# Performance work log

Hardware: AMD Instinct MI355X
Metric: run time of the kernel (lower is better)

The kernel has to match this reference:

```python
import jax, jax.numpy as jnp
import numpy as np

# dims
B, S, V, H, D, I, L, SL, P = 1, 2048, 32000, 1024, 512, 4096, 2, 32, 4096
DECAY_FAST, DECAY_SLOW, CONS_RATE, CONS_EVERY = 0.9, 0.99, 0.1, 10


def _ln(x, g, b):
    m = x.mean(-1, keepdims=True)
    v = ((x - m) ** 2).mean(-1, keepdims=True)
    return (x - m) * jax.lax.rsqrt(v + 1e-5) * g + b


def _memory_scan(items, gates, fast0, slow0):
    # items [B,S,D], gates [B,S,SL]; sequential per-timestep memory update
    cons = (jnp.arange(items.shape[1]) % CONS_EVERY) == 0
    def step(carry, x):
        fast, slow = carry
        item, gate, c = x
        fast = DECAY_FAST * fast + gate[:, :, None] * item[:, None, :]
        slow = jnp.where(c, DECAY_SLOW * slow + CONS_RATE * fast, slow)
        fast = jnp.where(c, (1.0 - CONS_RATE) * fast, fast)
        return (fast, slow), None
    (fast, slow), _ = jax.lax.scan(
        step, (fast0, slow0),
        (items.transpose(1, 0, 2), gates.transpose(1, 0, 2), cons))
    return fast, slow


def _forward(input_ids, fast_states, slow_states, emb, pos_emb, W_item, b_item,
             W_q, b_q, rh_W1, rh_b1, rh_W2, rh_b2, gate_W, gate_b, W_out, b_out,
             ln1_g, ln1_b, ffn_W1, ffn_b1, ffn_W2, ffn_b2, ln2_g, ln2_b, fln_g, fln_b):
    b, s = input_ids.shape
    h = emb[input_ids] + pos_emb[:s][None]  # [B,S,H]
    new_fast, new_slow = [], []
    for l in range(W_item.shape[0]):
        items = h @ W_item[l] + b_item[l]          # [B,S,D]
        query = h @ W_q[l] + b_q[l]                # [B,S,H]
        # retrieval head -> unit-norm unbinding keys
        k1 = jax.nn.gelu(items @ rh_W1[l] + rh_b1[l])
        keys = k1 @ rh_W2[l] + rh_b2[l]
        keys = keys / (jnp.linalg.norm(keys, axis=-1, keepdims=True) + 1e-6)
        fast0, slow0 = fast_states[l], slow_states[l]  # [B,SL,D]
        # retrieval uses the initial (constant-within-sequence) states, so it
        # vectorizes over seq: slot attention + hadamard unbinding
        mem = jnp.concatenate([fast0, slow0], axis=1)  # [B,2*SL,D]
        scores = jnp.einsum('bsd,bnd->bsn', keys, mem) / jnp.sqrt(jnp.float32(D))
        attn = jax.nn.softmax(scores, axis=-1)
        retrieved = jnp.einsum('bsn,bnd->bsd', attn, mem) * keys  # [B,S,D]
        gates = jax.nn.sigmoid(jnp.concatenate([h, retrieved], -1) @ gate_W[l] + gate_b[l])
        fast_gates = gates[..., :SL]
        fast, slow = _memory_scan(items, fast_gates, fast0, slow0)
        new_fast.append(fast)
        new_slow.append(slow)
        out = jnp.concatenate([query, retrieved], -1) @ W_out[l] + b_out[l]
        h = _ln(h + out, ln1_g[l], ln1_b[l])
        ffn = jax.nn.gelu(h @ ffn_W1[l] + ffn_b1[l]) @ ffn_W2[l] + ffn_b2[l]
        h = _ln(h + ffn, ln2_g[l], ln2_b[l])
    h = _ln(h, fln_g, fln_b)
    logits = jnp.einsum('bsh,vh->bsv', h, emb)  # tied lm_head
    return logits, jnp.stack(new_fast), jnp.stack(new_slow)


def setup_inputs() -> dict:
    key = jax.random.key(0)
    def rn(i, shape, scale=0.02):
        return jax.random.normal(jax.random.fold_in(key, i), shape, dtype=jnp.float32) * scale
    z = lambda shape: jnp.zeros(shape, jnp.float32)
    return dict(
        input_ids=jax.random.randint(jax.random.fold_in(key, 0), (B, S), 0, V),
        fast_states=rn(100, (L, B, SL, D), 0.5),
        slow_states=rn(101, (L, B, SL, D), 0.5),
        emb=rn(1, (V, H)),
        pos_emb=rn(2, (P, H)),
        W_item=rn(3, (L, H, D)), b_item=z((L, D)),
        W_q=rn(4, (L, H, H)), b_q=z((L, H)),
        rh_W1=rn(5, (L, D, 2 * D)), rh_b1=z((L, 2 * D)),
        rh_W2=rn(6, (L, 2 * D, D)), rh_b2=z((L, D)),
        gate_W=rn(7, (L, H + D, 2 * SL)), gate_b=z((L, 2 * SL)),
        W_out=rn(8, (L, H + D, H)), b_out=z((L, H)),
        ln1_g=jnp.ones((L, H)), ln1_b=z((L, H)),
        ffn_W1=rn(9, (L, H, I)), ffn_b1=z((L, I)),
        ffn_W2=rn(10, (L, I, H)), ffn_b2=z((L, H)),
        ln2_g=jnp.ones((L, H)), ln2_b=z((L, H)),
        fln_g=jnp.ones((H,)), fln_b=z((H,)),
    )


def reference(input_ids, fast_states, slow_states, emb, pos_emb, W_item, b_item,
              W_q, b_q, rh_W1, rh_b1, rh_W2, rh_b2, gate_W, gate_b, W_out, b_out,
              ln1_g, ln1_b, ffn_W1, ffn_b1, ffn_W2, ffn_b2, ln2_g, ln2_b, fln_g, fln_b):
    return _forward(input_ids, fast_states, slow_states, emb, pos_emb, W_item, b_item,
                    W_q, b_q, rh_W1, rh_b1, rh_W2, rh_b2, gate_W, gate_b, W_out, b_out,
                    ln1_g, ln1_b, ffn_W1, ffn_b1, ffn_W2, ffn_b2, ln2_g, ln2_b, fln_g, fln_b)
```

## Files before the change

kernel.cpp:

```cpp
#include <hip/hip_runtime.h>
#include <hip/hip_bf16.h>
#include <stdint.h>

typedef __hip_bfloat16 bf16;
typedef float f32x4 __attribute__((ext_vector_type(4)));
typedef short s16x8 __attribute__((ext_vector_type(8)));
typedef short s16x4 __attribute__((ext_vector_type(4)));

#define DEV __device__ __forceinline__

static constexpr int S_ = 2048, H_ = 1024, D_ = 512, I_ = 4096, V_ = 32000;
static constexpr int SLn = 32, Lc = 2;
static constexpr size_t LOGITS_N = (size_t)S_ * V_;

DEV float gelu_f(float x) {
    float x3 = x * x * x;
    return 0.5f * x * (1.f + tanhf(0.7978845608028654f * (x + 0.044715f * x3)));
}

#define AS1(p) ((const __attribute__((address_space(1))) void*)(uintptr_t)(p))
#define AS3(p) ((__attribute__((address_space(3))) void*)(uint32_t)(uintptr_t)(p))

template <int BM, int BN, int TH, int WM, int WN, int FLAGS>
__global__ __launch_bounds__(TH, (TH == 512) ? 2 : 3) void gemm_p5(
    const bf16* __restrict__ A, int lda, const bf16* __restrict__ BT,
    const float* __restrict__ bias, float* __restrict__ Cf, int ldf,
    bf16* __restrict__ Cb, int ldb2, int K, int Mt, int Nt) {
    constexpr int FM = BM / (WM * 16), FN = BN / (WN * 16);
    constexpr int CA = (BM * 4) / TH, CB = (BN * 4) / TH, CH = CA + CB;
    constexpr int NPH = (FM * FN >= 32) ? 2 : 1;
    constexpr int FMP = FM / NPH;
    constexpr int BUFS = (BM + BN) * 32;
    __shared__ short lds[4 * BUFS];
    const int tid = threadIdx.x, lane = tid & 63;
    const int wm = (tid >> 6) / WN, wn = (tid >> 6) % WN;

    int nwg = Mt * Nt;
    int bid = blockIdx.x, wgid = bid;
    if ((nwg & 7) == 0) {
        int cpx = nwg >> 3;
        wgid = (bid & 7) * cpx + (bid >> 3);
    }
    const int m0 = (wgid % Mt) * BM, n0 = (wgid / Mt) * BN;

    const bf16* aS[CA];
    const bf16* bS[CB];
#pragma unroll
    for (int c = 0; c < CA; ++c) {
        int L = (c * TH + tid) * 16;
        int sidx = L >> 10, w = L & 1023;
        int r16 = w >> 6;
        int c2 = (w & 63) ^ (((r16 >> 3) & 1) << 5);
        aS[c] = A + (size_t)(m0 + sidx * 16 + r16) * lda + (c2 >> 1);
    }
#pragma unroll
    for (int c = 0; c < CB; ++c) {
        int L = (c * TH + tid) * 16;
        int sidx = L >> 10, w = L & 1023;
        int r16 = w >> 6;
        int c2 = (w & 63) ^ (((r16 >> 3) & 1) << 5);
        bS[c] = BT + (size_t)(n0 + sidx * 16 + r16) * K + (c2 >> 1);
    }

    auto stageA = [&](int kt) {
        short* dst = &lds[(kt & 3) * BUFS];
#pragma unroll
        for (int c = 0; c < CA; ++c)
            __builtin_amdgcn_global_load_lds(AS1(aS[c] + kt * 32), AS3(dst + (c * TH + tid) * 8), 16, 0, 0);
    };
    auto stageB = [&](int kt) {
        short* dst = &lds[(kt & 3) * BUFS + BM * 32];
#pragma unroll
        for (int c = 0; c < CB; ++c)
            __builtin_amdgcn_global_load_lds(AS1(bS[c] + kt * 32), AS3(dst + (c * TH + tid) * 8), 16, 0, 0);
    };

    const int laneoff = ((lane & 15) * 64 + ((((lane >> 4) * 8) ^ (((lane >> 3) & 1) << 4)) << 1)) >> 1;

    f32x4 acc[FM][FN];
#pragma unroll
    for (int i = 0; i < FM; i++)
#pragma unroll
        for (int j = 0; j < FN; j++)
#pragma unroll
            for (int r = 0; r < 4; r++) acc[i][j][r] = 0.f;

    const int NT = K >> 5;
    stageA(0); stageB(0);
    stageA(1); stageB(1);
    stageA(2); stageB(2);
    asm volatile("s_waitcnt vmcnt(%0)" ::"n"(2 * CH) : "memory");
    __builtin_amdgcn_s_barrier();

    for (int t = 0; t < NT; ++t) {
        const short* as = &lds[(t & 3) * BUFS];
        const short* bs = as + BM * 32;
        s16x8 bf[FN];
#pragma unroll
        for (int p = 0; p < NPH; ++p) {
            s16x8 af[FMP];
#pragma unroll
            for (int i = 0; i < FMP; i++)
                af[i] = *(const s16x8*)&as[(wm * FM + p * FMP + i) * 512 + laneoff];
            if (p == 0) {
#pragma unroll
                for (int j = 0; j < FN; j++)
                    bf[j] = *(const s16x8*)&bs[(wn * FN + j) * 512 + laneoff];
            }
            if (t + 3 < NT) {
                if (NPH == 1) {
                    stageA(t + 3);
                    stageB(t + 3);
                } else if (p == 0) {
                    stageA(t + 3);
                } else {
                    stageB(t + 3);
                }
            }
            if (p == NPH - 1 && t + 1 < NT) {
                const int ahead = NT - 2 - t;
                if (ahead >= 2)
                    asm volatile("s_waitcnt vmcnt(%0)" ::"n"(2 * CH) : "memory");
                else if (ahead == 1)
                    asm volatile("s_waitcnt vmcnt(%0)" ::"n"(CH) : "memory");
                else
                    asm volatile("s_waitcnt vmcnt(0)" ::: "memory");
            }
            __builtin_amdgcn_s_barrier();
            __builtin_amdgcn_sched_barrier(0);
            __builtin_amdgcn_s_setprio(1);
#pragma unroll
            for (int i = 0; i < FMP; i++)
#pragma unroll
                for (int j = 0; j < FN; j++)
                    acc[p * FMP + i][j] =
                        __builtin_amdgcn_mfma_f32_16x16x32_bf16(af[i], bf[j], acc[p * FMP + i][j], 0, 0, 0);
            __builtin_amdgcn_s_setprio(0);
            __builtin_amdgcn_s_barrier();
        }
    }

#pragma unroll
    for (int i = 0; i < FM; i++) {
        int gr0 = m0 + (wm * FM + i) * 16 + ((lane >> 4) << 2);
#pragma unroll
        for (int j = 0; j < FN; j++) {
            int gc = n0 + (wn * FN + j) * 16 + (lane & 15);
            float bv = (FLAGS & 1) ? bias[gc] : 0.f;
#pragma unroll
            for (int r = 0; r < 4; r++) {
                float v = acc[i][j][r] + bv;
                if (FLAGS & 2) v = gelu_f(v);
                if (FLAGS & 4) Cf[(size_t)(gr0 + r) * ldf + gc] = v;
                if (FLAGS & 8) Cb[(size_t)(gr0 + r) * ldb2 + gc] = __float2bfloat16(v);
            }
        }
    }
}

__global__ __launch_bounds__(256) void transpose_bf16_kernel(const float* __restrict__ W,
                                                             bf16* __restrict__ WT, int K, int N) {
    __shared__ float t[32][33];
    int tx = threadIdx.x & 31, ty = threadIdx.x >> 5;
    int kb = blockIdx.y * 32, nb = blockIdx.x * 32;
#pragma unroll
    for (int i = 0; i < 4; i++)
        t[ty + 8 * i][tx] = W[(size_t)(kb + ty + 8 * i) * N + nb + tx];
    __syncthreads();
#pragma unroll
    for (int i = 0; i < 4; i++)
        WT[(size_t)(nb + ty + 8 * i) * K + kb + tx] = __float2bfloat16(t[tx][ty + 8 * i]);
}

__global__ void conv_bf16_kernel(const float* __restrict__ src, bf16* __restrict__ dst) {
    size_t i = (size_t)blockIdx.x * 256 + threadIdx.x;
    f32x4 v = ((const f32x4*)src)[i];
    s16x4 o;
#pragma unroll
    for (int j = 0; j < 4; j++) {
        bf16 h = __float2bfloat16(v[j]);
        o[j] = *(short*)&h;
    }
    ((s16x4*)dst)[i] = o;
}

__global__ void embed_kernel(const int* __restrict__ ids, const float* __restrict__ emb,
                             const float* __restrict__ pos, float* __restrict__ hF,
                             bf16* __restrict__ hB) {
    int t = blockIdx.x, tid = threadIdx.x;
    int id = ids[t];
    f32x4 v = ((const f32x4*)(emb + (size_t)id * H_))[tid];
    f32x4 q = ((const f32x4*)(pos + (size_t)t * H_))[tid];
    v = v + q;
    ((f32x4*)(hF + (size_t)t * H_))[tid] = v;
    s16x4 o;
#pragma unroll
    for (int j = 0; j < 4; j++) {
        bf16 h = __float2bfloat16(v[j]);
        o[j] = *(short*)&h;
    }
    ((s16x4*)(hB + (size_t)t * 1536))[tid] = o;
}

__global__ __launch_bounds__(256) void ln_kernel(const float* __restrict__ x,
                                                 const float* __restrict__ res,
                                                 const float* __restrict__ g,
                                                 const float* __restrict__ b,
                                                 float* __restrict__ of, bf16* __restrict__ ob,
                                                 int ldo) {
    __shared__ float red[8];
    int row = blockIdx.x, tid = threadIdx.x, lane = tid & 63, wid = tid >> 6;
    const float* xr = x + (size_t)row * H_;
    float v[4];
#pragma unroll
    for (int j = 0; j < 4; j++) {
        int c = tid + 256 * j;
        v[j] = xr[c] + (res ? res[(size_t)row * H_ + c] : 0.f);
    }
    float s = v[0] + v[1] + v[2] + v[3];
#pragma unroll
    for (int o = 32; o; o >>= 1) s += __shfl_xor(s, o);
    if (!lane) red[wid] = s;
    __syncthreads();
    float mean = (red[0] + red[1] + red[2] + red[3]) * (1.f / H_);
    float q = 0.f;
#pragma unroll
    for (int j = 0; j < 4; j++) {
        float d = v[j] - mean;
        q += d * d;
    }
#pragma unroll
    for (int o = 32; o; o >>= 1) q += __shfl_xor(q, o);
    if (!lane) red[4 + wid] = q;
    __syncthreads();
    float var = (red[4] + red[5] + red[6] + red[7]) * (1.f / H_);
    float rstd = rsqrtf(var + 1e-5f);
#pragma unroll
    for (int j = 0; j < 4; j++) {
        int c = tid + 256 * j;
        float o2 = (v[j] - mean) * rstd * g[c] + b[c];
        if (of) of[(size_t)row * H_ + c] = o2;
        if (ob) ob[(size_t)row * ldo + c] = __float2bfloat16(o2);
    }
}

__global__ void memt_kernel(const float* __restrict__ fast0, const float* __restrict__ slow0,
                            float* __restrict__ memT) {
    int idx = blockIdx.x * 256 + threadIdx.x;
    int d = idx >> 6, n = idx & 63;
    const float* m = (n < 32) ? fast0 + (size_t)n * D_ : slow0 + (size_t)(n - 32) * D_;
    memT[idx] = m[d];
}

__global__ __launch_bounds__(256) void attn_kernel(const float* __restrict__ keys,
                                                   const float* __restrict__ memT,
                                                   const float* __restrict__ fast0,
                                                   const float* __restrict__ slow0,
                                                   bf16* __restrict__ qr, bf16* __restrict__ hr) {
    __shared__ float klds[4][512];
    int wid = threadIdx.x >> 6, lane = threadIdx.x & 63;
    int r = blockIdx.x * 4 + wid;
    float kv[8], ss = 0.f;
#pragma unroll
    for (int j = 0; j < 8; j++) {
        kv[j] = keys[(size_t)r * D_ + lane + 64 * j];
        ss += kv[j] * kv[j];
    }
#pragma unroll
    for (int o = 32; o; o >>= 1) ss += __shfl_xor(ss, o);
    float inv = 1.f / (sqrtf(ss) + 1e-6f);
#pragma unroll
    for (int j = 0; j < 8; j++) {
        kv[j] *= inv;
        klds[wid][lane + 64 * j] = kv[j];
    }
    __syncthreads();
    float s0 = 0.f, s1 = 0.f, s2 = 0.f, s3 = 0.f;
#pragma unroll 8
    for (int d = 0; d < 512; d += 4) {
        s0 = fmaf(klds[wid][d + 0], memT[(d + 0) * 64 + lane], s0);
        s1 = fmaf(klds[wid][d + 1], memT[(d + 1) * 64 + lane], s1);
        s2 = fmaf(klds[wid][d + 2], memT[(d + 2) * 64 + lane], s2);
        s3 = fmaf(klds[wid][d + 3], memT[(d + 3) * 64 + lane], s3);
    }
    float s = (s0 + s1 + s2 + s3) * 0.044194173824159216f;
    float m = s;
#pragma unroll
    for (int o = 32; o; o >>= 1) m = fmaxf(m, __shfl_xor(m, o));
    float p = expf(s - m);
    float sum = p;
#pragma unroll
    for (int o = 32; o; o >>= 1) sum += __shfl_xor(sum, o);
    float pn = p / sum;
    float rv[8];
#pragma unroll
    for (int j = 0; j < 8; j++) rv[j] = 0.f;
    for (int n2 = 0; n2 < 64; ++n2) {
        float a2 = __shfl(pn, n2);
        const float* m2 = (n2 < 32) ? (fast0 + (size_t)n2 * D_) : (slow0 + (size_t)(n2 - 32) * D_);
#pragma unroll
        for (int j = 0; j < 8; j++) rv[j] = fmaf(a2, m2[lane + 64 * j], rv[j]);
    }
#pragma unroll
    for (int j = 0; j < 8; j++) {
        bf16 o = __float2bfloat16(rv[j] * kv[j]);
        qr[(size_t)r * 1536 + 1024 + lane + 64 * j] = o;
        hr[(size_t)r * 1536 + 1024 + lane + 64 * j] = o;
    }
}

__global__ void coef_kernel(float* __restrict__ coef) {
    int t = blockIdx.x * 256 + threadIdx.x;
    int j0 = (t + 9) / 10;
    float a = powf(0.9f, (float)(2047 - t + 205 - j0));
    float b = 0.f;
    for (int j = j0; j < 205; ++j)
        b += powf(0.9f, (float)(10 * j - t + j - j0)) * powf(0.99f, (float)(204 - j));
    b *= 0.1f;
    coef[t] = a;
    coef[2048 + t] = b;
    if (t == 0) {
        coef[4096] = powf(0.99f, 205.f);
        float cfs = 0.f;
        for (int j = 0; j < 205; ++j)
            cfs += powf(0.9f, (float)(11 * j + 1)) * powf(0.99f, (float)(204 - j));
        coef[4097] = 0.1f * cfs;
    }
}

__global__ void sigcoef_kernel(const float* __restrict__ raw, const float* __restrict__ coef,
                               float* __restrict__ ga, float* __restrict__ gb) {
    int i = blockIdx.x * 256 + threadIdx.x;
    int r = i >> 5, n = i & 31;
    float g = 1.f / (1.f + expf(-raw[r * 64 + n]));
    ga[i] = g * coef[r];
    gb[i] = g * coef[2048 + r];
}

__global__ __launch_bounds__(256) void scan_part_kernel(const float* __restrict__ items,
                                                        const float* __restrict__ ga,
                                                        const float* __restrict__ gb,
                                                        float* __restrict__ pF,
                                                        float* __restrict__ pS) {
    int tid = threadIdx.x;
    int d = (blockIdx.x & 7) * 64 + (tid & 63);
    int mg = (blockIdx.x >> 3) & 1;
    int tc = blockIdx.x >> 4;
    int m0 = mg * 16 + (tid >> 6) * 4;
    float aF[4] = {0.f, 0.f, 0.f, 0.f}, aS[4] = {0.f, 0.f, 0.f, 0.f};
    for (int t = tc * 128; t < tc * 128 + 128; ++t) {
        float it = items[(size_t)t * D_ + d];
#pragma unroll
        for (int j = 0; j < 4; j++) {
            aF[j] = fmaf(ga[t * 32 + m0 + j], it, aF[j]);
            aS[j] = fmaf(gb[t * 32 + m0 + j], it, aS[j]);
        }
    }
#pragma unroll
    for (int j = 0; j < 4; j++) {
        pF[((size_t)tc * 32 + m0 + j) * D_ + d] = aF[j];
        pS[((size_t)tc * 32 + m0 + j) * D_ + d] = aS[j];
    }
}

__global__ __launch_bounds__(256) void scan_reduce_kernel(const float* __restrict__ pF,
                                                          const float* __restrict__ pS,
                                                          const float* __restrict__ coef,
                                                          const float* __restrict__ fast0,
                                                          const float* __restrict__ slow0,
                                                          float* __restrict__ fastO,
                                                          float* __restrict__ slowO) {
    int i = blockIdx.x * 256 + threadIdx.x;
    float f = 0.f, s = 0.f;
#pragma unroll
    for (int c = 0; c < 16; c++) {
        f += pF[(size_t)c * 32 * D_ + i];
        s += pS[(size_t)c * 32 * D_ + i];
    }
    fastO[i] = f;
    slowO[i] = s + coef[4096] * slow0[i] + coef[4097] * fast0[i];
}

static inline void gemmM(hipStream_t st, const bf16* A, int lda, const bf16* BT,
                         const float* bias, float* Cf, int ldf, bf16* Cb, int ldb2,
                         int M, int N, int K, int flags) {
    int Mt = M / 128, Nt = N / 64;
    dim3 g(Mt * Nt), b(256);
#define GCASE(fl)                                                                             \
    if (flags == fl) {                                                                        \
        gemm_p5<128, 64, 256, 2, 2, fl><<<g, b, 0, st>>>(A, lda, BT, bias, Cf, ldf, Cb, ldb2, \
                                                         K, Mt, Nt);                          \
        return;                                                                               \
    }
    GCASE(13)
    GCASE(9)
    GCASE(11)
    GCASE(5)
#undef GCASE
}

static inline void transp(hipStream_t st, const float* W, bf16* WT, int K, int N) {
    transpose_bf16_kernel<<<dim3(N / 32, K / 32), 256, 0, st>>>(W, WT, K, N);
}

extern "C" void kernel_launch(void* const* d_in, const int* in_sizes, int n_in,
                              void* d_out, int out_size, void* d_ws, size_t ws_size,
                              hipStream_t stream) {
    const int* ids = (const int*)d_in[0];
    const float* fastS = (const float*)d_in[1];
    const float* slowS = (const float*)d_in[2];
    const float* emb = (const float*)d_in[3];
    const float* pos = (const float*)d_in[4];
    const float* W_item = (const float*)d_in[5];
    const float* b_item = (const float*)d_in[6];
    const float* W_q = (const float*)d_in[7];
    const float* b_q = (const float*)d_in[8];
    const float* rh_W1 = (const float*)d_in[9];
    const float* rh_b1 = (const float*)d_in[10];
    const float* rh_W2 = (const float*)d_in[11];
    const float* rh_b2 = (const float*)d_in[12];
    const float* gate_W = (const float*)d_in[13];
    const float* gate_b = (const float*)d_in[14];
    const float* W_out = (const float*)d_in[15];
    const float* b_out = (const float*)d_in[16];
    const float* ln1_g = (const float*)d_in[17];
    const float* ln1_b = (const float*)d_in[18];
    const float* ffn_W1 = (const float*)d_in[19];
    const float* ffn_b1 = (const float*)d_in[20];
    const float* ffn_W2 = (const float*)d_in[21];
    const float* ffn_b2 = (const float*)d_in[22];
    const float* ln2_g = (const float*)d_in[23];
    const float* ln2_b = (const float*)d_in[24];
    const float* fln_g = (const float*)d_in[25];
    const float* fln_b = (const float*)d_in[26];
    float* outP = (float*)d_out;

    size_t off = 0;
    char* base = (char*)d_ws;
    auto alloc = [&](size_t n) -> char* {
        char* p = base + off;
        off += (n + 255) & ~(size_t)255;
        return p;
    };
    bf16* wItemT = (bf16*)alloc((size_t)Lc * D_ * H_ * 2);
    bf16* wQT = (bf16*)alloc((size_t)Lc * H_ * H_ * 2);
    bf16* rh1T = (bf16*)alloc((size_t)Lc * (2 * D_) * D_ * 2);
    bf16* rh2T = (bf16*)alloc((size_t)Lc * D_ * (2 * D_) * 2);
    bf16* wOutT = (bf16*)alloc((size_t)Lc * H_ * 1536 * 2);
    bf16* f1T = (bf16*)alloc((size_t)Lc * I_ * H_ * 2);
    bf16* f2T = (bf16*)alloc((size_t)Lc * H_ * I_ * 2);
    bf16* gWT = (bf16*)alloc((size_t)Lc * 64 * 1536 * 2);
    bf16* embB = (bf16*)alloc((size_t)V_ * H_ * 2);
    float* hF = (float*)alloc((size_t)S_ * H_ * 4);
    bf16* hrB = (bf16*)alloc((size_t)S_ * 1536 * 2);
    bf16* hB = hrB;
    float* itemsF = (float*)alloc((size_t)S_ * D_ * 4);
    bf16* itemsB = (bf16*)alloc((size_t)S_ * D_ * 2);
    bf16* qrB = (bf16*)alloc((size_t)S_ * 1536 * 2);
    bf16* k1B = (bf16*)alloc((size_t)S_ * (2 * D_) * 2);
    float* keysF = (float*)alloc((size_t)S_ * D_ * 4);
    float* outF = (float*)alloc((size_t)S_ * H_ * 4);
    bf16* ffn1B = (bf16*)alloc((size_t)S_ * I_ * 2);
    float* gRawF = (float*)alloc((size_t)S_ * 64 * 4);
    float* gaF = (float*)alloc((size_t)S_ * SLn * 4);
    float* gbF = (float*)alloc((size_t)S_ * SLn * 4);
    float* coefF = (float*)alloc(4200 * 4);
    float* memT = (float*)alloc((size_t)D_ * 64 * 4);
    float* pF = (float*)alloc((size_t)16 * SLn * D_ * 4);
    float* pS = (float*)alloc((size_t)16 * SLn * D_ * 4);

    coef_kernel<<<8, 256, 0, stream>>>(coefF);
    for (int l = 0; l < Lc; ++l) {
        transp(stream, W_item + (size_t)l * H_ * D_, wItemT + (size_t)l * D_ * H_, H_, D_);
        transp(stream, W_q + (size_t)l * H_ * H_, wQT + (size_t)l * H_ * H_, H_, H_);
        transp(stream, rh_W1 + (size_t)l * D_ * 2 * D_, rh1T + (size_t)l * 2 * D_ * D_, D_, 2 * D_);
        transp(stream, rh_W2 + (size_t)l * 2 * D_ * D_, rh2T + (size_t)l * D_ * 2 * D_, 2 * D_, D_);
        transp(stream, W_out + (size_t)l * 1536 * H_, wOutT + (size_t)l * H_ * 1536, 1536, H_);
        transp(stream, ffn_W1 + (size_t)l * H_ * I_, f1T + (size_t)l * I_ * H_, H_, I_);
        transp(stream, ffn_W2 + (size_t)l * I_ * H_, f2T + (size_t)l * H_ * I_, I_, H_);
        transp(stream, gate_W + (size_t)l * 1536 * 64, gWT + (size_t)l * 64 * 1536, 1536, 64);
    }
    conv_bf16_kernel<<<(int)((size_t)V_ * H_ / 4 / 256), 256, 0, stream>>>(emb, embB);
    embed_kernel<<<S_, 256, 0, stream>>>(ids, emb, pos, hF, hB);

    for (int l = 0; l < Lc; ++l) {
        const float* fast0 = fastS + (size_t)l * SLn * D_;
        const float* slow0 = slowS + (size_t)l * SLn * D_;
        gemmM(stream, hB, 1536, wItemT + (size_t)l * D_ * H_, b_item + l * D_, itemsF, D_,
              itemsB, D_, S_, D_, H_, 13);
        gemmM(stream, hB, 1536, wQT + (size_t)l * H_ * H_, b_q + l * H_, nullptr, 0, qrB, 1536,
              S_, H_, H_, 9);
        gemmM(stream, itemsB, D_, rh1T + (size_t)l * 2 * D_ * D_, rh_b1 + l * 2 * D_, nullptr, 0,
              k1B, 2 * D_, S_, 2 * D_, D_, 11);
        gemmM(stream, k1B, 2 * D_, rh2T + (size_t)l * D_ * 2 * D_, rh_b2 + l * D_, keysF, D_,
              nullptr, 0, S_, D_, 2 * D_, 5);
        memt_kernel<<<128, 256, 0, stream>>>(fast0, slow0, memT);
        attn_kernel<<<S_ / 4, 256, 0, stream>>>(keysF, memT, fast0, slow0, qrB, hrB);
        gemmM(stream, hrB, 1536, gWT + (size_t)l * 64 * 1536, gate_b + l * 64, gRawF, 64,
              nullptr, 0, S_, 64, 1536, 5);
        sigcoef_kernel<<<S_ * SLn / 256, 256, 0, stream>>>(gRawF, coefF, gaF, gbF);
        scan_part_kernel<<<256, 256, 0, stream>>>(itemsF, gaF, gbF, pF, pS);
        scan_reduce_kernel<<<64, 256, 0, stream>>>(
            pF, pS, coefF, fast0, slow0, outP + LOGITS_N + (size_t)l * SLn * D_,
            outP + LOGITS_N + (size_t)Lc * SLn * D_ + (size_t)l * SLn * D_);
        gemmM(stream, qrB, 1536, wOutT + (size_t)l * H_ * 1536, b_out + l * H_, outF, H_,
              nullptr, 0, S_, H_, 1536, 5);
        ln_kernel<<<S_, 256, 0, stream>>>(hF, outF, ln1_g + l * H_, ln1_b + l * H_, hF, hB, 1536);
        gemmM(stream, hB, 1536, f1T + (size_t)l * I_ * H_, ffn_b1 + l * I_, nullptr, 0, ffn1B,
              I_, S_, I_, H_, 11);
        gemmM(stream, ffn1B, I_, f2T + (size_t)l * H_ * I_, ffn_b2 + l * H_, outF, H_, nullptr,
              0, S_, H_, I_, 5);
        ln_kernel<<<S_, 256, 0, stream>>>(hF, outF, ln2_g + l * H_, ln2_b + l * H_, hF, hB, 1536);
    }
    ln_kernel<<<S_, 256, 0, stream>>>(hF, nullptr, fln_g, fln_b, nullptr, hB, 1536);
    gemm_p5<256, 256, 512, 2, 4, 4><<<1000, 512, 0, stream>>>(hB, 1536, embB, nullptr, outP, V_,
                                                              nullptr, 0, H_, 8, 125);
}
```

Measured before the change: 923.8 us.

## Fuse item/query projections and add dedicated register-A logits GEMM

Concatenates the transposed W_item and W_q into one weight so a single GEMM produces both items (fp32 and bf16) and query, with a split epilogue that routes columns to separate outputs. It also replaces the 256x256 logits GEMM with a dedicated 256x128 tile kernel that loads A fragments straight from global memory into double-buffered registers and stages only B through LDS. The vmcnt wait logic in the generic GEMM is adjusted, and its launch bounds now always request 3 waves per SIMD. The goals are fewer launches, better reuse of the shared input, and a lighter LDS load for the large vocabulary GEMM, at the cost of more register pressure and A reads that are not coalesced through LDS.

```diff
diff --git a/kernel.cpp b/kernel.cpp
--- a/kernel.cpp
+++ b/kernel.cpp
@@ -21,11 +21,110 @@
 #define AS1(p) ((const __attribute__((address_space(1))) void*)(uintptr_t)(p))
 #define AS3(p) ((__attribute__((address_space(3))) void*)(uint32_t)(uintptr_t)(p))
 
+__global__ __launch_bounds__(256, 2) void logits_gemm(const bf16* __restrict__ A,
+                                                      const bf16* __restrict__ BT,
+                                                      float* __restrict__ C) {
+    constexpr int NT = 32, SLOT = 128 * 32;
+    __shared__ short lds[4 * SLOT];
+    const int tid = threadIdx.x, lane = tid & 63;
+    const int wm = (tid >> 6) >> 1, wn = (tid >> 6) & 1;
+
+    int bid = blockIdx.x;
+    int wgid = (bid & 7) * 250 + (bid >> 3);
+    const int m0 = (wgid & 7) * 256;
+    const int n0 = (wgid >> 3) * 128;
+
+    const bf16* bS[2];
+#pragma unroll
+    for (int c = 0; c < 2; ++c) {
+        int L = (c * 256 + tid) * 16;
+        int sidx = L >> 10, w = L & 1023;
+        int r16 = w >> 6;
+        int c2 = (w & 63) ^ (((r16 >> 3) & 1) << 5);
+        bS[c] = BT + (size_t)(n0 + sidx * 16 + r16) * 1024 + (c2 >> 1);
+    }
+    auto stageB = [&](int kt) {
+        short* dst = &lds[(kt & 3) * SLOT];
+#pragma unroll
+        for (int c = 0; c < 2; ++c)
+            __builtin_amdgcn_global_load_lds(AS1(bS[c] + kt * 32), AS3(dst + (c * 256 + tid) * 8), 16, 0, 0);
+    };
+    const int laneoff = ((lane & 15) * 64 + ((((lane >> 4) * 8) ^ (((lane >> 3) & 1) << 4)) << 1)) >> 1;
+
+    const bf16* aP[8];
+#pragma unroll
+    for (int fi = 0; fi < 8; ++fi)
+        aP[fi] = A + (size_t)(m0 + wm * 128 + fi * 16 + (lane & 15)) * 1536 + ((lane >> 4) * 8);
+
+    f32x4 acc[8][4];
+#pragma unroll
+    for (int i = 0; i < 8; i++)
+#pragma unroll
+        for (int j = 0; j < 4; j++)
+#pragma unroll
+            for (int r = 0; r < 4; r++) acc[i][j][r] = 0.f;
+
+    s16x8 a0[8], a1[8];
+    stageB(0);
+    stageB(1);
+    stageB(2);
+#pragma unroll
+    for (int fi = 0; fi < 8; ++fi) a0[fi] = *(const s16x8*)(aP[fi]);
+    asm volatile("s_waitcnt vmcnt(0)" ::: "memory");
+    __builtin_amdgcn_s_barrier();
+
+    auto iter = [&](int t, s16x8(&cur)[8], s16x8(&nxt)[8]) {
+        const short* bs = &lds[(t & 3) * SLOT];
+        s16x8 bf[4];
+#pragma unroll
+        for (int j = 0; j < 4; ++j)
+            bf[j] = *(const s16x8*)&bs[(wn * 4 + j) * 512 + laneoff];
+        if (t + 1 < NT) {
+#pragma unroll
+            for (int fi = 0; fi < 8; ++fi) nxt[fi] = *(const s16x8*)(aP[fi] + (t + 1) * 32);
+        }
+        if (t >= 1 && t + 2 < NT) stageB(t + 2);
+        if (t + 2 < NT)
+            asm volatile("s_waitcnt vmcnt(10)" ::: "memory");
+        else if (t + 1 < NT)
+            asm volatile("s_waitcnt vmcnt(8)" ::: "memory");
+        else
+            asm volatile("s_waitcnt vmcnt(0)" ::: "memory");
+        asm volatile("s_waitcnt lgkmcnt(0)" ::: "memory");
+        __builtin_amdgcn_s_barrier();
+        __builtin_amdgcn_sched_barrier(0);
+        __builtin_amdgcn_s_setprio(1);
+#pragma unroll
+        for (int i = 0; i < 8; ++i)
+#pragma unroll
+            for (int j = 0; j < 4; ++j)
+                acc[i][j] = __builtin_amdgcn_mfma_f32_16x16x32_bf16(cur[i], bf[j], acc[i][j], 0, 0, 0);
+        __builtin_amdgcn_s_setprio(0);
+    };
+
+    for (int t = 0; t < NT; t += 2) {
+        iter(t, a0, a1);
+        iter(t + 1, a1, a0);
+    }
+
+#pragma unroll
+    for (int i = 0; i < 8; i++) {
+        int gr0 = m0 + (wm * 8 + i) * 16 + ((lane >> 4) << 2);
+#pragma unroll
+        for (int j = 0; j < 4; j++) {
+            int gc = n0 + (wn * 4 + j) * 16 + (lane & 15);
+#pragma unroll
+            for (int r = 0; r < 4; r++) C[(size_t)(gr0 + r) * V_ + gc] = acc[i][j][r];
+        }
+    }
+}
+
 template <int BM, int BN, int TH, int WM, int WN, int FLAGS>
-__global__ __launch_bounds__(TH, (TH == 512) ? 2 : 3) void gemm_p5(
+__global__ __launch_bounds__(TH, 3) void gemm_p5(
     const bf16* __restrict__ A, int lda, const bf16* __restrict__ BT,
-    const float* __restrict__ bias, float* __restrict__ Cf, int ldf,
-    bf16* __restrict__ Cb, int ldb2, int K, int Mt, int Nt) {
+    const float* __restrict__ bias, const float* __restrict__ bias2,
+    float* __restrict__ Cf, int ldf, bf16* __restrict__ Cb, int ldb2,
+    bf16* __restrict__ Cb2, int K, int Mt, int Nt) {
     constexpr int FM = BM / (WM * 16), FN = BN / (WN * 16);
     constexpr int CA = (BM * 4) / TH, CB = (BN * 4) / TH, CH = CA + CB;
     constexpr int NPH = (FM * FN >= 32) ? 2 : 1;
@@ -91,7 +190,6 @@
     stageA(2); stageB(2);
     asm volatile("s_waitcnt vmcnt(%0)" ::"n"(2 * CH) : "memory");
     __builtin_amdgcn_s_barrier();
-
     for (int t = 0; t < NT; ++t) {
         const short* as = &lds[(t & 3) * BUFS];
         const short* bs = as + BM * 32;
@@ -117,11 +215,11 @@
                     stageB(t + 3);
                 }
             }
-            if (p == NPH - 1 && t + 1 < NT) {
-                const int ahead = NT - 2 - t;
-                if (ahead >= 2)
+            if (p == NPH - 1) {
+                const int rem = NT - 1 - t;
+                if (rem >= 3)
                     asm volatile("s_waitcnt vmcnt(%0)" ::"n"(2 * CH) : "memory");
-                else if (ahead == 1)
+                else if (rem == 2)
                     asm volatile("s_waitcnt vmcnt(%0)" ::"n"(CH) : "memory");
                 else
                     asm volatile("s_waitcnt vmcnt(0)" ::: "memory");
@@ -146,13 +244,30 @@
 #pragma unroll
         for (int j = 0; j < FN; j++) {
             int gc = n0 + (wn * FN + j) * 16 + (lane & 15);
-            float bv = (FLAGS & 1) ? bias[gc] : 0.f;
-#pragma unroll
-            for (int r = 0; r < 4; r++) {
-                float v = acc[i][j][r] + bv;
-                if (FLAGS & 2) v = gelu_f(v);
-                if (FLAGS & 4) Cf[(size_t)(gr0 + r) * ldf + gc] = v;
-                if (FLAGS & 8) Cb[(size_t)(gr0 + r) * ldb2 + gc] = __float2bfloat16(v);
+            if (FLAGS & 32) {
+                if (n0 < 512) {
+                    float bv = bias[gc];
+#pragma unroll
+                    for (int r = 0; r < 4; r++) {
+                        float v = acc[i][j][r] + bv;
+                        Cf[(size_t)(gr0 + r) * 512 + gc] = v;
+                        Cb2[(size_t)(gr0 + r) * 512 + gc] = __float2bfloat16(v);
+                    }
+                } else {
+                    float bv = bias2[gc - 512];
+#pragma unroll
+                    for (int r = 0; r < 4; r++)
+                        Cb[(size_t)(gr0 + r) * 1536 + (gc - 512)] = __float2bfloat16(acc[i][j][r] + bv);
+                }
+            } else {
+                float bv = (FLAGS & 1) ? bias[gc] : 0.f;
+#pragma unroll
+                for (int r = 0; r < 4; r++) {
+                    float v = acc[i][j][r] + bv;
+                    if (FLAGS & 2) v = gelu_f(v);
+                    if (FLAGS & 4) Cf[(size_t)(gr0 + r) * ldf + gc] = v;
+                    if (FLAGS & 8) Cb[(size_t)(gr0 + r) * ldb2 + gc] = __float2bfloat16(v);
+                }
             }
         }
     }
@@ -382,18 +497,17 @@
 }
 
 static inline void gemmM(hipStream_t st, const bf16* A, int lda, const bf16* BT,
-                         const float* bias, float* Cf, int ldf, bf16* Cb, int ldb2,
-                         int M, int N, int K, int flags) {
+                         const float* bias, const float* bias2, float* Cf, int ldf, bf16* Cb,
+                         int ldb2, bf16* Cb2, int M, int N, int K, int flags) {
     int Mt = M / 128, Nt = N / 64;
     dim3 g(Mt * Nt), b(256);
-#define GCASE(fl)                                                                             \
-    if (flags == fl) {                                                                        \
-        gemm_p5<128, 64, 256, 2, 2, fl><<<g, b, 0, st>>>(A, lda, BT, bias, Cf, ldf, Cb, ldb2, \
-                                                         K, Mt, Nt);                          \
-        return;                                                                               \
-    }
-    GCASE(13)
-    GCASE(9)
+#define GCASE(fl)                                                                                  \
+    if (flags == fl) {                                                                             \
+        gemm_p5<128, 64, 256, 2, 2, fl><<<g, b, 0, st>>>(A, lda, BT, bias, bias2, Cf, ldf, Cb,     \
+                                                         ldb2, Cb2, K, Mt, Nt);                    \
+        return;                                                                                    \
+    }
+    GCASE(33)
     GCASE(11)
     GCASE(5)
 #undef GCASE
@@ -442,8 +556,7 @@
         off += (n + 255) & ~(size_t)255;
         return p;
     };
-    bf16* wItemT = (bf16*)alloc((size_t)Lc * D_ * H_ * 2);
-    bf16* wQT = (bf16*)alloc((size_t)Lc * H_ * H_ * 2);
+    bf16* wIQ = (bf16*)alloc((size_t)Lc * 1536 * H_ * 2);
     bf16* rh1T = (bf16*)alloc((size_t)Lc * (2 * D_) * D_ * 2);
     bf16* rh2T = (bf16*)alloc((size_t)Lc * D_ * (2 * D_) * 2);
     bf16* wOutT = (bf16*)alloc((size_t)Lc * H_ * 1536 * 2);
@@ -471,8 +584,9 @@
 
     coef_kernel<<<8, 256, 0, stream>>>(coefF);
     for (int l = 0; l < Lc; ++l) {
-        transp(stream, W_item + (size_t)l * H_ * D_, wItemT + (size_t)l * D_ * H_, H_, D_);
-        transp(stream, W_q + (size_t)l * H_ * H_, wQT + (size_t)l * H_ * H_, H_, H_);
+        transp(stream, W_item + (size_t)l * H_ * D_, wIQ + (size_t)l * 1536 * H_, H_, D_);
+        transp(stream, W_q + (size_t)l * H_ * H_, wIQ + (size_t)l * 1536 * H_ + (size_t)512 * H_,
+               H_, H_);
         transp(stream, rh_W1 + (size_t)l * D_ * 2 * D_, rh1T + (size_t)l * 2 * D_ * D_, D_, 2 * D_);
         transp(stream, rh_W2 + (size_t)l * 2 * D_ * D_, rh2T + (size_t)l * D_ * 2 * D_, 2 * D_, D_);
         transp(stream, W_out + (size_t)l * 1536 * H_, wOutT + (size_t)l * H_ * 1536, 1536, H_);
@@ -486,33 +600,30 @@
     for (int l = 0; l < Lc; ++l) {
         const float* fast0 = fastS + (size_t)l * SLn * D_;
         const float* slow0 = slowS + (size_t)l * SLn * D_;
-        gemmM(stream, hB, 1536, wItemT + (size_t)l * D_ * H_, b_item + l * D_, itemsF, D_,
-              itemsB, D_, S_, D_, H_, 13);
-        gemmM(stream, hB, 1536, wQT + (size_t)l * H_ * H_, b_q + l * H_, nullptr, 0, qrB, 1536,
-              S_, H_, H_, 9);
-        gemmM(stream, itemsB, D_, rh1T + (size_t)l * 2 * D_ * D_, rh_b1 + l * 2 * D_, nullptr, 0,
-              k1B, 2 * D_, S_, 2 * D_, D_, 11);
-        gemmM(stream, k1B, 2 * D_, rh2T + (size_t)l * D_ * 2 * D_, rh_b2 + l * D_, keysF, D_,
-              nullptr, 0, S_, D_, 2 * D_, 5);
+        gemmM(stream, hB, 1536, wIQ + (size_t)l * 1536 * H_, b_item + l * D_, b_q + l * H_,
+              itemsF, 512, qrB, 1536, itemsB, S_, 1536, H_, 33);
+        gemmM(stream, itemsB, D_, rh1T + (size_t)l * 2 * D_ * D_, rh_b1 + l * 2 * D_, nullptr,
+              nullptr, 0, k1B, 2 * D_, nullptr, S_, 2 * D_, D_, 11);
+        gemmM(stream, k1B, 2 * D_, rh2T + (size_t)l * D_ * 2 * D_, rh_b2 + l * D_, nullptr,
+              keysF, D_, nullptr, 0, nullptr, S_, D_, 2 * D_, 5);
         memt_kernel<<<128, 256, 0, stream>>>(fast0, slow0, memT);
         attn_kernel<<<S_ / 4, 256, 0, stream>>>(keysF, memT, fast0, slow0, qrB, hrB);
-        gemmM(stream, hrB, 1536, gWT + (size_t)l * 64 * 1536, gate_b + l * 64, gRawF, 64,
-              nullptr, 0, S_, 64, 1536, 5);
+        gemmM(stream, hrB, 1536, gWT + (size_t)l * 64 * 1536, gate_b + l * 64, nullptr, gRawF,
+              64, nullptr, 0, nullptr, S_, 64, 1536, 5);
         sigcoef_kernel<<<S_ * SLn / 256, 256, 0, stream>>>(gRawF, coefF, gaF, gbF);
         scan_part_kernel<<<256, 256, 0, stream>>>(itemsF, gaF, gbF, pF, pS);
         scan_reduce_kernel<<<64, 256, 0, stream>>>(
             pF, pS, coefF, fast0, slow0, outP + LOGITS_N + (size_t)l * SLn * D_,
             outP + LOGITS_N + (size_t)Lc * SLn * D_ + (size_t)l * SLn * D_);
-        gemmM(stream, qrB, 1536, wOutT + (size_t)l * H_ * 1536, b_out + l * H_, outF, H_,
-              nullptr, 0, S_, H_, 1536, 5);
+        gemmM(stream, qrB, 1536, wOutT + (size_t)l * H_ * 1536, b_out + l * H_, nullptr, outF,
+              H_, nullptr, 0, nullptr, S_, H_, 1536, 5);
         ln_kernel<<<S_, 256, 0, stream>>>(hF, outF, ln1_g + l * H_, ln1_b + l * H_, hF, hB, 1536);
-        gemmM(stream, hB, 1536, f1T + (size_t)l * I_ * H_, ffn_b1 + l * I_, nullptr, 0, ffn1B,
-              I_, S_, I_, H_, 11);
-        gemmM(stream, ffn1B, I_, f2T + (size_t)l * H_ * I_, ffn_b2 + l * H_, outF, H_, nullptr,
-              0, S_, H_, I_, 5);
+        gemmM(stream, hB, 1536, f1T + (size_t)l * I_ * H_, ffn_b1 + l * I_, nullptr, nullptr, 0,
+              ffn1B, I_, nullptr, S_, I_, H_, 11);
+        gemmM(stream, ffn1B, I_, f2T + (size_t)l * H_ * I_, ffn_b2 + l * H_, nullptr, outF, H_,
+              nullptr, 0, nullptr, S_, H_, I_, 5);
         ln_kernel<<<S_, 256, 0, stream>>>(hF, outF, ln2_g + l * H_, ln2_b + l * H_, hF, hB, 1536);
     }
     ln_kernel<<<S_, 256, 0, stream>>>(hF, nullptr, fln_g, fln_b, nullptr, hB, 1536);
-    gemm_p5<256, 256, 512, 2, 4, 4><<<1000, 512, 0, stream>>>(hB, 1536, embB, nullptr, outP, V_,
-                                                              nullptr, 0, H_, 8, 125);
-}
+    logits_gemm<<<2000, 256, 0, stream>>>(hB, embB, outP);
+}
```

Measured after the change: 1.031 ms. 11.6% more time.
